# Optimization experiments

Measured on AMD Instinct MI355X. Metric: run time of the kernel, lower is better.

Reference implementation:

```python
import jax, jax.numpy as jnp
import numpy as np

B, FEAT_DIM, GUIDE_DIM, NIR = 1, 128, 128, 33
HL, WL, HH, WH = 64, 64, 256, 256


def make_coord(h, w):
    # pixel-center coords in [-1,1], order (y, x) matching torch make_coord((h,w))
    ys = -1.0 + 1.0 / h + (2.0 / h) * jnp.arange(h, dtype=jnp.float32)
    xs = -1.0 + 1.0 / w + (2.0 / w) * jnp.arange(w, dtype=jnp.float32)
    yy, xx = jnp.meshgrid(ys, xs, indexing='ij')
    return jnp.stack([yy, xx], axis=-1)  # [h, w, 2]


def grid_sample_nearest(img, coord):
    # img [B,C,Hi,Wi]; coord [B,N,2] normalized (y,x).
    # Matches F.grid_sample(mode='nearest', align_corners=False, padding_mode='zeros')
    # (torch passes coord.flip(-1), i.e. (x,y); we index (y,x) directly -- equivalent).
    Bb, C, Hi, Wi = img.shape
    y, x = coord[..., 0], coord[..., 1]
    iy = jnp.round((y + 1.0) * Hi / 2.0 - 0.5).astype(jnp.int32)
    ix = jnp.round((x + 1.0) * Wi / 2.0 - 0.5).astype(jnp.int32)
    valid = (iy >= 0) & (iy < Hi) & (ix >= 0) & (ix < Wi)
    idx = jnp.clip(iy, 0, Hi - 1) * Wi + jnp.clip(ix, 0, Wi - 1)  # [B,N]
    g = jnp.take_along_axis(img.reshape(Bb, C, Hi * Wi), idx[:, None, :], axis=2)
    g = jnp.where(valid[:, None, :], g, 0.0)
    return jnp.transpose(g, (0, 2, 1))  # [B,N,C]


def depthwise3x3(x, k):
    C = x.shape[1]
    return jax.lax.conv_general_dilated(x, k[:, None, :, :], (1, 1), ((1, 1), (1, 1)),
                                        feature_group_count=C,
                                        dimension_numbers=('NCHW', 'OIHW', 'NCHW'))


def query_freq(feat, coord, hr_guide, mlp_fn):
    # local-ensemble implicit decode (query_freq_a / query_freq_p share this skeleton)
    b, c, h, w = feat.shape
    H, W = hr_guide.shape[-2], hr_guide.shape[-1]
    coord = jnp.broadcast_to(coord, (b, H * W, 2))
    fcoord = jnp.broadcast_to(jnp.transpose(make_coord(h, w), (2, 0, 1))[None], (b, 2, h, w))
    q_guide = grid_sample_nearest(hr_guide, coord)  # [b,N,Cg]
    rx, ry = 1.0 / h, 1.0 / w
    hw = jnp.array([float(h), float(w)], dtype=coord.dtype)
    preds = []
    for vx in (-1.0, 1.0):
        for vy in (-1.0, 1.0):
            c_ = coord + jnp.array([vx * rx, vy * ry], dtype=coord.dtype)
            q_feat = grid_sample_nearest(feat, c_)    # [b,N,Cf]
            q_coord = grid_sample_nearest(fcoord, c_)  # [b,N,2]
            rel = (coord - q_coord) * hw
            inp = jnp.concatenate([q_feat, q_guide, rel], axis=-1)  # [b,N,Cin]
            preds.append(mlp_fn(inp, H, W))  # [b,N,NIR]
    preds = jnp.stack(preds, axis=-1)  # [b,N,NIR,4]
    weight = jax.nn.softmax(preds[:, :, -1, :], axis=-1)  # [b,N,4]
    ret = jnp.sum(preds[:, :, :-1, :] * weight[:, :, None, :], axis=-1)  # [b,N,NIR-1]
    return jnp.transpose(ret, (0, 2, 1)).reshape(b, -1, H, W)


def fourier_unit(feat, coord, hr_guide, w1a, b1a, w2a, b2a, w3a, b3a,
                 pw1, dw1, pw2, dw2, pw3, dw3):
    def mlp_a(inp, H, W):  # plain MLP (imnet1)
        x = jax.nn.relu(inp @ w1a + b1a)
        x = jax.nn.relu(x @ w2a + b2a)
        return x @ w3a + b3a

    def mlp_p(inp, H, W):  # conv MLP (imnet2 / MLP_P)
        b = inp.shape[0]
        x = inp.reshape(b, -1, H, W)  # faithful to torch .view on [B,N,Cin]
        x = jax.nn.relu(depthwise3x3(jnp.einsum('bchw,oc->bohw', x, pw1), dw1))
        x = jax.nn.relu(depthwise3x3(jnp.einsum('bchw,oc->bohw', x, pw2), dw2))
        x = depthwise3x3(jnp.einsum('bchw,oc->bohw', x, pw3), dw3)
        return x.reshape(b, H * W, -1)  # faithful to torch .view(B,N,-1)

    feat_f = jnp.fft.fftn(feat, axes=(-2, -1))
    guide_f = jnp.fft.fftn(hr_guide, axes=(-2, -1))
    mag = query_freq(jnp.abs(feat_f), coord, jnp.abs(guide_f), mlp_a)
    pha = query_freq(jnp.angle(feat_f), coord, jnp.angle(guide_f), mlp_p)
    ffted = jax.lax.complex(mag * jnp.cos(pha), mag * jnp.sin(pha))
    return jnp.abs(jnp.fft.ifftn(ffted, axes=(-2, -1)))


def setup_inputs() -> dict:
    key = jax.random.key(0)
    ks = jax.random.split(key, 12)
    cin = FEAT_DIM + GUIDE_DIM + 2  # 258

    def lin(k, i, o):
        return jax.random.normal(k, (i, o), jnp.float32) / np.float32(np.sqrt(i))

    return dict(
        feat=jax.random.normal(ks[0], (B, FEAT_DIM, HL, WL), jnp.float32),
        coord=make_coord(HH, WH).reshape(1, HH * WH, 2),
        hr_guide=jax.random.normal(ks[1], (B, GUIDE_DIM, HH, WH), jnp.float32),
        w1a=lin(ks[2], cin, 256), b1a=jnp.zeros((256,), jnp.float32),
        w2a=lin(ks[3], 256, 128), b2a=jnp.zeros((128,), jnp.float32),
        w3a=lin(ks[4], 128, NIR), b3a=jnp.zeros((NIR,), jnp.float32),
        pw1=jax.random.normal(ks[5], (256, cin), jnp.float32) / np.float32(np.sqrt(cin)),
        dw1=jax.random.normal(ks[6], (256, 3, 3), jnp.float32) / np.float32(3.0),
        pw2=jax.random.normal(ks[7], (128, 256), jnp.float32) / np.float32(16.0),
        dw2=jax.random.normal(ks[8], (128, 3, 3), jnp.float32) / np.float32(3.0),
        pw3=jax.random.normal(ks[9], (NIR, 128), jnp.float32) / np.float32(np.sqrt(128.0)),
        dw3=jax.random.normal(ks[10], (NIR, 3, 3), jnp.float32) / np.float32(3.0),
    )


def reference(feat, coord, hr_guide, w1a, b1a, w2a, b2a, w3a, b3a,
              pw1, dw1, pw2, dw2, pw3, dw3):
    return fourier_unit(feat, coord, hr_guide, w1a, b1a, w2a, b2a, w3a, b3a,
                        pw1, dw1, pw2, dw2, pw3, dw3)
```

## Files before the change

### kernel.cpp

```cpp
#include <hip/hip_runtime.h>
#include <math.h>

typedef __attribute__((ext_vector_type(4))) float f32x4;
typedef __attribute__((ext_vector_type(8))) short bf16x8;
typedef _Float16 f16x8 __attribute__((ext_vector_type(8)));
typedef _Float16 f16x4 __attribute__((ext_vector_type(4)));

__device__ __forceinline__ short f2bf(float v) {
    union { float f; unsigned u; } x; x.f = v;
    unsigned r = x.u + 0x7FFF + ((x.u >> 16) & 1);
    return (short)(r >> 16);
}
__device__ __forceinline__ float bf2f(short b) {
    union { unsigned u; float f; } x; x.u = ((unsigned)(unsigned short)b) << 16;
    return x.f;
}
__device__ __forceinline__ short f2h(float v) {
    union { _Float16 h; short s; } u; u.h = (_Float16)v; return u.s;
}
__device__ __forceinline__ void gload16(const void* g, void* l) {
    __builtin_amdgcn_global_load_lds((const __attribute__((address_space(1))) void*)g,
                                     (__attribute__((address_space(3))) void*)l, 16, 0, 0);
}

template<int N, int MODE>
__global__ __launch_bounds__(256)
void fft_lines(const float* __restrict__ in_real, const float* __restrict__ in_pha,
               const float2* __restrict__ in_c, float2* __restrict__ out_c,
               int nlines, int lpp, int plane_stride, int line_pitch, int stride,
               float sgn, float scale)
{
    constexpr int H = N / 2;
    constexpr int LPB = 256 / H;
    __shared__ float2 bufA[LPB][N];
    __shared__ float2 bufB[LPB][N];
    __shared__ float2 W[H];
    const int tid = threadIdx.x;
    const int sub = tid / H;
    const int b   = tid % H;
    const int L   = blockIdx.x * LPB + sub;
    if (tid < H) {
        float ang = (6.283185307179586f / N) * tid;
        float s, c; sincosf(ang, &s, &c);
        W[tid] = make_float2(c, sgn * s);
    }
    const bool active = (L < nlines);
    size_t base = 0;
    if (active) {
        int p = L / lpp, q = L - p * lpp;
        base = (size_t)p * plane_stride + (size_t)q * line_pitch;
        if (MODE == 0) {
            bufA[sub][b]     = make_float2(in_real[base + (size_t)b * stride], 0.f);
            bufA[sub][b + H] = make_float2(in_real[base + (size_t)(b + H) * stride], 0.f);
        } else if (MODE == 1) {
            bufA[sub][b]     = in_c[base + (size_t)b * stride];
            bufA[sub][b + H] = in_c[base + (size_t)(b + H) * stride];
        } else {
            float m0 = in_real[base + (size_t)b * stride];
            float p0 = in_pha [base + (size_t)b * stride];
            float m1 = in_real[base + (size_t)(b + H) * stride];
            float p1 = in_pha [base + (size_t)(b + H) * stride];
            float s0, c0, s1, c1;
            sincosf(p0, &s0, &c0);
            sincosf(p1, &s1, &c1);
            bufA[sub][b]     = make_float2(m0 * c0, m0 * s0);
            bufA[sub][b + H] = make_float2(m1 * c1, m1 * s1);
        }
    }
    __syncthreads();
    float2 (*X)[N] = bufA;
    float2 (*Y)[N] = bufB;
    int m = 1;
    #pragma unroll
    for (int l = H; l >= 1; l >>= 1) {
        int jm = b & ~(m - 1);
        float2 c0 = X[sub][b];
        float2 c1 = X[sub][b + H];
        float2 w  = W[jm];
        float2 s0 = make_float2(c0.x + c1.x, c0.y + c1.y);
        float2 d  = make_float2(c0.x - c1.x, c0.y - c1.y);
        float2 t  = make_float2(d.x * w.x - d.y * w.y, d.x * w.y + d.y * w.x);
        Y[sub][b + jm]     = s0;
        Y[sub][b + jm + m] = t;
        __syncthreads();
        float2 (*tmp)[N] = X; X = Y; Y = tmp;
        m <<= 1;
    }
    if (active) {
        float2 r0 = X[sub][b], r1 = X[sub][b + H];
        out_c[base + (size_t)b * stride]       = make_float2(r0.x * scale, r0.y * scale);
        out_c[base + (size_t)(b + H) * stride] = make_float2(r1.x * scale, r1.y * scale);
    }
}

template<int N, int TC, int ABSOUT>
__global__ __launch_bounds__(256)
void fft_cols(const float2* __restrict__ in, float2* __restrict__ outc,
              float* __restrict__ outr, float sgn, float scale)
{
    constexpr int Q     = N / 4;
    constexpr int LOG4  = (N == 64) ? 3 : 4;
    constexpr int PITCH = ((N + N / 8 - 8 + 31) / 32) * 32 + 8;
    constexpr int ELD   = (N * TC) / 256;
    constexpr int EBF   = (Q * TC) / 256;
    static_assert((Q * TC) % 256 == 0, "butterfly count must fill block");
    __shared__ float bRe[2][TC * PITCH];
    __shared__ float bIm[2][TC * PITCH];
    __shared__ float Wre[Q + Q / 8 + 1];
    __shared__ float Wim[Q + Q / 8 + 1];
    const int tid = threadIdx.x;
    const int plane = blockIdx.y;
    const int c0 = blockIdx.x * TC;
    const size_t pbase = (size_t)plane * N * N + c0;
    auto lidx = [](int cc, int row) { return cc * PITCH + row + (row >> 3); };

    if (tid < Q) {
        float ang = (6.283185307179586f / N) * tid;
        float s, c; sincosf(ang, &s, &c);
        int wi = tid + (tid >> 3);
        Wre[wi] = c; Wim[wi] = sgn * s;
    }
    #pragma unroll
    for (int e = 0; e < ELD; e++) {
        int q = tid + e * 256;
        int r = q / TC, cc = q % TC;
        float2 v = in[pbase + (size_t)r * N + cc];
        int li = lidx(cc, r);
        bRe[0][li] = v.x; bIm[0][li] = v.y;
    }
    __syncthreads();
    int cur = 0, m = 1;
    #pragma unroll
    for (int stage = 0; stage < LOG4; stage++) {
        #pragma unroll
        for (int e = 0; e < EBF; e++) {
            int idx = tid + e * 256;
            int b = idx % Q, cc = idx / Q;
            int jm = b & ~(m - 1);
            int base = 3 * jm + b;
            int i0 = lidx(cc, b),         i1 = lidx(cc, b + Q);
            int i2 = lidx(cc, b + 2 * Q), i3 = lidx(cc, b + 3 * Q);
            float x0r = bRe[cur][i0], x0i = bIm[cur][i0];
            float x1r = bRe[cur][i1], x1i = bIm[cur][i1];
            float x2r = bRe[cur][i2], x2i = bIm[cur][i2];
            float x3r = bRe[cur][i3], x3i = bIm[cur][i3];
            int wi = jm + (jm >> 3);
            float w1r = Wre[wi], w1i = Wim[wi];
            float w2r = w1r * w1r - w1i * w1i, w2i = 2.f * w1r * w1i;
            float w3r = w2r * w1r - w2i * w1i, w3i = w2r * w1i + w2i * w1r;
            float ar = x0r + x2r, ai = x0i + x2i;
            float br = x0r - x2r, bi = x0i - x2i;
            float cr = x1r + x3r, ci = x1i + x3i;
            float dr = x1r - x3r, di = x1i - x3i;
            float edr = -sgn * di, edi = sgn * dr;
            float y0r = ar + cr,  y0i = ai + ci;
            float y1r = br + edr, y1i = bi + edi;
            float y2r = ar - cr,  y2i = ai - ci;
            float y3r = br - edr, y3i = bi - edi;
            int o0 = lidx(cc, base),         o1 = lidx(cc, base + m);
            int o2 = lidx(cc, base + 2 * m), o3 = lidx(cc, base + 3 * m);
            bRe[cur ^ 1][o0] = y0r;                     bIm[cur ^ 1][o0] = y0i;
            bRe[cur ^ 1][o1] = y1r * w1r - y1i * w1i;   bIm[cur ^ 1][o1] = y1r * w1i + y1i * w1r;
            bRe[cur ^ 1][o2] = y2r * w2r - y2i * w2i;   bIm[cur ^ 1][o2] = y2r * w2i + y2i * w2r;
            bRe[cur ^ 1][o3] = y3r * w3r - y3i * w3i;   bIm[cur ^ 1][o3] = y3r * w3i + y3i * w3r;
        }
        __syncthreads();
        cur ^= 1; m <<= 2;
    }
    #pragma unroll
    for (int e = 0; e < ELD; e++) {
        int q = tid + e * 256;
        int r = q / TC, cc = q % TC;
        int li = lidx(cc, r);
        float vr = bRe[cur][li], vi = bIm[cur][li];
        if (ABSOUT) {
            outr[pbase + (size_t)r * N + cc] = scale * sqrtf(vr * vr + vi * vi);
        } else {
            outc[pbase + (size_t)r * N + cc] = make_float2(vr * scale, vi * scale);
        }
    }
}

__global__ __launch_bounds__(256)
void extract_t(const float2* __restrict__ Fc, short* __restrict__ fAbf,
               short* __restrict__ fPH)
{
    __shared__ float2 T[128][17];
    const int tid = threadIdx.x;
    const int o0 = blockIdx.x * 16;
    #pragma unroll
    for (int e = 0; e < 8; e++) {
        int q = tid + e * 256;
        int c = q >> 4, oo = q & 15;
        T[c][oo] = Fc[(size_t)c * 4096 + o0 + oo];
    }
    __syncthreads();
    #pragma unroll
    for (int e = 0; e < 8; e++) {
        int q = tid + e * 256;
        int oo = q >> 7, c = q & 127;
        float2 v = T[c][oo];
        size_t idx = (size_t)(o0 + oo) * 128 + c;
        fAbf[idx] = f2bf(sqrtf(v.x * v.x + v.y * v.y));
        fPH[idx]  = f2h(atan2f(v.y, v.x));
    }
}

__global__ __launch_bounds__(256)
void gbuild_t(const float2* __restrict__ E, short* __restrict__ Ga,
              short* __restrict__ Gph)
{
    __shared__ float2 T[128][17];
    const int tid = threadIdx.x;
    const int n0 = blockIdx.x * 16;
    #pragma unroll
    for (int e = 0; e < 8; e++) {
        int q = tid + e * 256;
        int c = q >> 4, nn = q & 15;
        T[c][nn] = E[(size_t)c * 65536 + n0 + nn];
    }
    __syncthreads();
    #pragma unroll
    for (int e = 0; e < 8; e++) {
        int q = tid + e * 256;
        int nn = q >> 7, c = q & 127;
        float2 v = T[c][nn];
        size_t o = (size_t)(n0 + nn) * 128 + c;
        Ga[o]  = f2bf(sqrtf(v.x * v.x + v.y * v.y));
        Gph[o] = f2h(atan2f(v.y, v.x));
    }
}

__global__ __launch_bounds__(256)
void mag_h1(const short* __restrict__ FA1, const short* __restrict__ H1g,
            const float* __restrict__ w1a, const float* __restrict__ b1a,
            short* __restrict__ h1, int s0)
{
    int t = blockIdx.x * 256 + threadIdx.x;
    int n = t >> 5, oc = (t & 31) * 8;
    int im = n >> 16, nl = n & 65535;
    int s = s0 + im;
    int oy = (s < 2) ? -3 : 5;
    int ox = (s & 1) ? 5 : -3;
    int i = nl >> 8, jx = nl & 255;
    int iy = (2 * i + oy) >> 3;
    int ix = (2 * jx + ox) >> 3;
    bool valid = (iy >= 0 && iy < 64 && ix >= 0 && ix < 64);
    float ry = valid ? (0.5f * i - 2.f * iy - 0.75f) : (0.5f * i - 63.75f);
    float rx = valid ? (0.5f * jx - 2.f * ix - 0.75f) : (0.5f * jx - 63.75f);
    bf16x8 hv = *(const bf16x8*)&H1g[(size_t)nl * 256 + oc];
    bf16x8 fv = {};
    if (valid) fv = *(const bf16x8*)&FA1[(size_t)(iy * 64 + ix) * 256 + oc];
    bf16x8 out;
    #pragma unroll
    for (int k = 0; k < 8; k++) {
        int o = oc + k;
        float v = b1a[o] + bf2f(hv[k]) + ry * w1a[128 * 256 + o] + rx * w1a[129 * 256 + o];
        if (valid) v += bf2f(fv[k]);
        out[k] = f2bf(fmaxf(v, 0.f));
    }
    *(bf16x8*)&h1[(size_t)n * 256 + oc] = out;
}

__global__ __launch_bounds__(256)
void bphase_tile(const short* __restrict__ featPH, const short* __restrict__ Gph,
                 short* __restrict__ Xp, int s0)
{
    __shared__ short lds[64 * 146];
    const int tid = threadIdx.x;
    const int sh = blockIdx.x >> 11;
    const int inner = blockIdx.x & 2047;
    const int s = s0 + sh;
    const int oy = (s < 2) ? -3 : 5;
    const int ox = (s & 1) ? 5 : -3;
    const int p0 = (inner >> 1) * 64;
    const int half = inner & 1;
    const int pl = tid & 63;
    const int p = p0 + pl;
    const int jq = tid >> 6;
    unsigned* out32 = (unsigned*)Xp + (size_t)sh * 65536 * 144;
    int j = half * 144 + jq;
    unsigned f0 = (unsigned)j * 65536u + (unsigned)p;
    unsigned n = f0 / 258u;
    int c = (int)(f0 - n * 258u);
    #pragma unroll 4
    for (int e = 0; e < 36; e++) {
        short hv = 0;
        if (j < 258) {
            int i = (int)(n >> 8), jx = (int)(n & 255);
            int iy = (2 * i + oy) >> 3;
            int ix = (2 * jx + ox) >> 3;
            bool valid = (iy >= 0 && iy < 64 && ix >= 0 && ix < 64);
            if (c < 128) {
                hv = valid ? featPH[(size_t)(iy * 64 + ix) * 128 + c] : (short)0;
            } else if (c < 256) {
                hv = Gph[(size_t)n * 128 + (c - 128)];
            } else {
                float fv;
                if (c == 256) fv = valid ? (0.5f * i - 2.f * iy - 0.75f) : (0.5f * i - 63.75f);
                else          fv = valid ? (0.5f * jx - 2.f * ix - 0.75f) : (0.5f * jx - 63.75f);
                hv = f2h(fv);
            }
        }
        lds[pl * 146 + (j - half * 144)] = hv;
        j += 4; n += 1016; c += 16;
        if (c >= 258) { c -= 258; n += 1; }
    }
    __syncthreads();
    const unsigned* lds32 = (const unsigned*)lds;
    int pw = tid / 72, dw = tid - pw * 72;
    #pragma unroll 4
    for (int e = 0; e < 18; e++) {
        out32[(size_t)(p0 + pw) * 144 + half * 72 + dw] = lds32[pw * 73 + dw];
        pw += 3; dw += 40;
        if (dw >= 72) { dw -= 72; pw += 1; }
    }
}

__global__ void wprep_T(const float* __restrict__ src, short* __restrict__ dst,
                        int Ncols, int Nd, int Kp, int k0, int kn, int kr0, int krn)
{
    int t = blockIdx.x * 256 + threadIdx.x;
    if (t >= Nd * Kp) return;
    int o = t / Kp, j = t - o * Kp;
    int c = (j < kn) ? (k0 + j) : ((j < kn + krn) ? (kr0 + j - kn) : -1);
    float v = 0.f;
    if (c >= 0 && o < Ncols) v = src[(size_t)c * Ncols + o];
    dst[t] = f2bf(v);
}
__global__ void wprep_f16(const float* __restrict__ src, short* __restrict__ dst,
                          int Nsrc, int Ksrc, int Nd, int Kp, int kn)
{
    int t = blockIdx.x * 256 + threadIdx.x;
    if (t >= Nd * Kp) return;
    int o = t / Kp, j = t - o * Kp;
    float v = 0.f;
    if (j < kn && o < Nsrc) v = src[(size_t)o * Ksrc + j];
    dst[t] = f2h(v);
}

template<int RELU, int BIAS, int CIN, int OUTT, int F16>
__global__ __launch_bounds__(256)
void gemm_mfma(const short* __restrict__ A, const short* __restrict__ Bt,
               const float* __restrict__ bias, const void* __restrict__ Cin,
               void* __restrict__ Cout,
               int K, int Apitch, int Bpitch, int ldc, int Nout)
{
    __shared__ short As[4096];
    __shared__ short Bs[4096];
    const int tid = threadIdx.x;
    const int wave = tid >> 6, lane = tid & 63;
    const int bm = blockIdx.y * 128, bn = blockIdx.x * 128;
    const int wr = wave >> 1, wc = wave & 1;
    const int srow = wave * 32 + (lane >> 2);
    const int scol = (lane & 3) * 8;
    const int ldsoff = srow * 32 + scol;
    f32x4 acc[4][4] = {};
    const int ks_n = K >> 5;
    for (int ks = 0; ks < ks_n; ks++) {
        const int k0 = ks << 5;
        const short* gA = A + (size_t)(bm + srow) * Apitch + k0 + scol;
        gload16(gA, &As[ldsoff]);
        gload16(gA + 16 * Apitch, &As[ldsoff + 512]);
        const short* gB = Bt + (size_t)(bn + srow) * Bpitch + k0 + scol;
        gload16(gB, &Bs[ldsoff]);
        gload16(gB + 16 * Bpitch, &Bs[ldsoff + 512]);
        __syncthreads();
        const int fr = lane & 15;
        const int kreg = (lane >> 4) << 3;
        bf16x8 ah[4], bh[4];
        #pragma unroll
        for (int m = 0; m < 4; m++)
            ah[m] = *(const bf16x8*)&As[(wr * 64 + m * 16 + fr) * 32 + kreg];
        #pragma unroll
        for (int n = 0; n < 4; n++)
            bh[n] = *(const bf16x8*)&Bs[(wc * 64 + n * 16 + fr) * 32 + kreg];
        #pragma unroll
        for (int m = 0; m < 4; m++)
            #pragma unroll
            for (int n = 0; n < 4; n++) {
                if constexpr (F16)
                    acc[m][n] = __builtin_amdgcn_mfma_f32_16x16x32_f16(
                        __builtin_bit_cast(f16x8, ah[m]),
                        __builtin_bit_cast(f16x8, bh[n]), acc[m][n], 0, 0, 0);
                else
                    acc[m][n] = __builtin_amdgcn_mfma_f32_16x16x32_bf16(
                        ah[m], bh[n], acc[m][n], 0, 0, 0);
            }
        __syncthreads();
    }
    const int fr = lane & 15;
    const int rg = (lane >> 4) * 4;
    #pragma unroll
    for (int n = 0; n < 4; n++) {
        const int col = bn + wc * 64 + n * 16 + fr;
        if (col >= Nout) continue;
        const float bv = BIAS ? bias[col] : 0.f;
        #pragma unroll
        for (int m = 0; m < 4; m++) {
            const int row0 = bm + wr * 64 + m * 16 + rg;
            #pragma unroll
            for (int r = 0; r < 4; r++) {
                float v = acc[m][n][r] + bv;
                const size_t ci = (size_t)(row0 + r) * ldc + col;
                if (CIN == 1) v += bf2f(((const short*)Cin)[ci]);
                if (RELU) v = fmaxf(v, 0.f);
                if constexpr (OUTT == 1)      ((float*)Cout)[ci] = v;
                else if constexpr (OUTT == 2) ((_Float16*)Cout)[ci] = (_Float16)v;
                else                          ((short*)Cout)[ci] = f2bf(v);
            }
        }
    }
}

template<int C, int RELU>
__global__ __launch_bounds__(256)
void dwconv_f16(const _Float16* __restrict__ in, const float* __restrict__ w,
                _Float16* __restrict__ out)
{
    constexpr int CG = C / 4;
    constexpr int SUBS = 256 / CG;
    constexpr int PX = SUBS * 2;
    const int tid = threadIdx.x;
    const int cg = tid % CG;
    const int c4 = cg * 4;
    const int sub = tid / CG;
    const int p0 = blockIdx.x * PX + sub * 2;
    const int im = p0 >> 16;
    const int pl = p0 & 65535;
    const int y = pl >> 8, x0 = pl & 255;
    const size_t ibase = (size_t)im * 65536 * C;
    float wk[4][9];
    #pragma unroll
    for (int k = 0; k < 4; k++)
        #pragma unroll
        for (int q = 0; q < 9; q++) wk[k][q] = w[(c4 + k) * 9 + q];
    f16x4 v[3][4];
    #pragma unroll
    for (int dy = 0; dy < 3; dy++) {
        int yy = y + dy - 1;
        bool yv = (yy >= 0) && (yy <= 255);
        int yc = min(max(yy, 0), 255);
        #pragma unroll
        for (int dx = 0; dx < 4; dx++) {
            int xx = x0 + dx - 1;
            bool xv = (xx >= 0) && (xx <= 255);
            int xc = min(max(xx, 0), 255);
            f16x4 t = *(const f16x4*)&in[ibase + (size_t)(yc * 256 + xc) * C + c4];
            v[dy][dx] = (yv && xv) ? t : (f16x4){};
        }
    }
    float a0[4] = {}, a1[4] = {};
    #pragma unroll
    for (int dy = 0; dy < 3; dy++)
        #pragma unroll
        for (int dx = 0; dx < 3; dx++)
            #pragma unroll
            for (int k = 0; k < 4; k++) {
                a0[k] += (float)v[dy][dx][k]     * wk[k][dy * 3 + dx];
                a1[k] += (float)v[dy][dx + 1][k] * wk[k][dy * 3 + dx];
            }
    f16x4 o0, o1;
    #pragma unroll
    for (int k = 0; k < 4; k++) {
        float b0 = RELU ? fmaxf(a0[k], 0.f) : a0[k];
        float b1 = RELU ? fmaxf(a1[k], 0.f) : a1[k];
        o0[k] = (_Float16)b0;
        o1[k] = (_Float16)b1;
    }
    *(f16x4*)&out[(size_t)p0 * C + c4]       = o0;
    *(f16x4*)&out[(size_t)(p0 + 1) * C + c4] = o1;
}

__global__ __launch_bounds__(256)
void dwconv3_t(const float* __restrict__ in, const float* __restrict__ w,
               float* __restrict__ out)
{
    __shared__ float lds[33][65];
    const int tid = threadIdx.x;
    const int im = blockIdx.x >> 10;
    const int inner = blockIdx.x & 1023;
    const int y = inner >> 2;
    const int x0 = (inner & 3) * 64;
    const size_t ibase = (size_t)im * 65536 * 33;
    const size_t obase = (size_t)im * 65536 * 33;
    #pragma unroll
    for (int e = 0; e < 9; e++) {
        int q = e * 256 + tid;
        if (q < 2112) {
            int x = q / 33, c = q - x * 33;
            float acc = 0.f;
            #pragma unroll
            for (int dy = 0; dy < 3; dy++) {
                int yy = y + dy - 1;
                bool yv = (yy >= 0) && (yy <= 255);
                int yc = min(max(yy, 0), 255);
                #pragma unroll
                for (int dx = 0; dx < 3; dx++) {
                    int xx = x0 + x + dx - 1;
                    bool xv = (xx >= 0) && (xx <= 255);
                    int xc = min(max(xx, 0), 255);
                    float t = in[ibase + (size_t)(yc * 256 + xc) * 33 + c];
                    acc += ((yv && xv) ? t : 0.f) * w[c * 9 + dy * 3 + dx];
                }
            }
            lds[c][x] = acc;
        }
    }
    __syncthreads();
    const int xx = tid & 63, c4 = tid >> 6;
    #pragma unroll
    for (int cg = 0; cg < 36; cg += 4) {
        int cc = cg + c4;
        if (cc < 33)
            out[obase + (size_t)cc * 65536 + y * 256 + x0 + xx] = lds[cc][xx];
    }
}

__global__ __launch_bounds__(256)
void ensemble_a(const short* __restrict__ P, float* __restrict__ mag)
{
    int n = blockIdx.x * 256 + threadIdx.x;
    float w[4]; float mx = -1e30f;
    #pragma unroll
    for (int s = 0; s < 4; s++) {
        w[s] = bf2f(P[((size_t)s * 65536 + n) * 33 + 32]);
        mx = fmaxf(mx, w[s]);
    }
    float sum = 0.f;
    #pragma unroll
    for (int s = 0; s < 4; s++) { w[s] = expf(w[s] - mx); sum += w[s]; }
    float inv = 1.f / sum;
    for (int ch = 0; ch < 32; ch++) {
        float a = 0.f;
        #pragma unroll
        for (int s = 0; s < 4; s++)
            a += bf2f(P[((size_t)s * 65536 + n) * 33 + ch]) * w[s];
        mag[(size_t)ch * 65536 + n] = a * inv;
    }
}

__global__ __launch_bounds__(256)
void ensemble_p(const float* __restrict__ P, float* __restrict__ pha)
{
    const size_t SOFF = (size_t)65536 * 33;
    int n = blockIdx.x * 256 + threadIdx.x;
    const size_t base = (size_t)n * 33;
    float w[4]; float mx = -1e30f;
    #pragma unroll
    for (int s = 0; s < 4; s++) {
        w[s] = P[(size_t)s * SOFF + base + 32];
        mx = fmaxf(mx, w[s]);
    }
    float sum = 0.f;
    #pragma unroll
    for (int s = 0; s < 4; s++) { w[s] = expf(w[s] - mx); sum += w[s]; }
    float inv = 1.f / sum;
    for (int jj = 0; jj < 32; jj++) {
        float a = 0.f;
        #pragma unroll
        for (int s = 0; s < 4; s++)
            a += P[(size_t)s * SOFF + base + jj] * w[s];
        pha[(size_t)jj * 65536 + n] = a * inv;
    }
}

extern "C" void kernel_launch(void* const* d_in, const int* in_sizes, int n_in,
                              void* d_out, int out_size, void* d_ws, size_t ws_size,
                              hipStream_t stream)
{
    (void)in_sizes; (void)n_in; (void)out_size; (void)ws_size;
    const float* feat = (const float*)d_in[0];
    const float* hr   = (const float*)d_in[2];
    const float* w1a  = (const float*)d_in[3];
    const float* b1a  = (const float*)d_in[4];
    const float* w2a  = (const float*)d_in[5];
    const float* b2a  = (const float*)d_in[6];
    const float* w3a  = (const float*)d_in[7];
    const float* b3a  = (const float*)d_in[8];
    const float* pw1  = (const float*)d_in[9];
    const float* dw1  = (const float*)d_in[10];
    const float* pw2  = (const float*)d_in[11];
    const float* dw2  = (const float*)d_in[12];
    const float* pw3  = (const float*)d_in[13];
    const float* dw3  = (const float*)d_in[14];

    char* W = (char*)d_ws;
    const size_t oA = 0;
    const size_t oB = 75497472;
    const size_t oC = oB + 67108864;
    const size_t oD = oC + 33554432;
    const size_t oM = oD + 34603008;
    const size_t oF = oM + 12582912;
    const size_t oN = oF + 786432;

    float2* E     = (float2*)(W + oA);
    short*  h1_2  = (short*) (W + oA);
    short*  Xp2   = (short*) (W + oA);
    _Float16* X2_2 = (_Float16*)(W + oA);
    float*  C3_2  = (float*) (W + oA);
    float*  Hp    = (float*) (W + oA);
    float2* Fc    = (float2*)(W + oB);
    short*  Ga    = (short*) (W + oB);
    short*  h2_2  = (short*) (W + oB);
    short*  H1g   = (short*) (W + oB + 33554432);
    _Float16* C1_2 = (_Float16*)(W + oB);
    _Float16* C2_2 = (_Float16*)(W + oB);
    _Float16* X3_2 = (_Float16*)(W + oB + 33554432);
    float2* Z     = (float2*)(W + oB);
    short*  Gph   = (short*) (W + oC);
    short*  PA    = (short*) (W + oD);
    float*  PP    = (float*) (W + oD);
    short*  featPH = (short*)(W + oM);
    float*  Hm     = (float*)(W + oM + 4194304);
    short* W1g = (short*)(W + oF + 81920);
    short* W2  = (short*)(W + oF + 147456);
    short* W3  = (short*)(W + oF + 212992);
    short* Pf  = (short*)(W + oF + 245760);
    short* P2  = (short*)(W + oF + 393216);
    short* P3  = (short*)(W + oF + 458752);
    short* W1a128 = (short*)(W + oF + 491520);
    short* featAbf = (short*)(W + oN);
    short* FA1     = (short*)(W + oN + 1048576);

    const size_t SOFF = (size_t)65536 * 33;

    wprep_T<<<128, 256, 0, stream>>>(w1a, W1a128, 256, 256, 128, 0, 128, 0, 0);
    wprep_T<<<128, 256, 0, stream>>>(w1a, W1g, 256, 256, 128, 128, 128, 0, 0);
    wprep_T<<<128, 256, 0, stream>>>(w2a, W2, 128, 128, 256, 0, 256, 0, 0);
    wprep_T<<<64,  256, 0, stream>>>(w3a, W3, 33, 128, 128, 0, 128, 0, 0);
    wprep_f16<<<288, 256, 0, stream>>>(pw1, Pf, 256, 258, 256, 288, 258);
    wprep_f16<<<128, 256, 0, stream>>>(pw2, P2, 128, 256, 128, 256, 256);
    wprep_f16<<<64,  256, 0, stream>>>(pw3, P3, 33, 128, 128, 128, 128);

    fft_lines<256, 0><<<16384, 256, 0, stream>>>(hr, nullptr, nullptr, E, 32768, 256, 65536, 256, 1, -1.f, 1.f);
    fft_cols<256, 8, 0><<<dim3(32, 128), 256, 0, stream>>>(E, E, nullptr, -1.f, 1.f);
    fft_lines<64, 0><<<1024, 256, 0, stream>>>(feat, nullptr, nullptr, Fc, 8192, 64, 4096, 64, 1, -1.f, 1.f);
    fft_cols<64, 16, 0><<<dim3(4, 128), 256, 0, stream>>>(Fc, Fc, nullptr, -1.f, 1.f);
    extract_t<<<256, 256, 0, stream>>>(Fc, featAbf, featPH);

    gbuild_t<<<4096, 256, 0, stream>>>(E, Ga, Gph);

    gemm_mfma<0,0,0,0,0><<<dim3(2,512), 256, 0, stream>>>(Ga, W1g, nullptr, nullptr, H1g, 128, 128, 128, 256, 256);
    gemm_mfma<0,0,0,0,0><<<dim3(2,32), 256, 0, stream>>>(featAbf, W1a128, nullptr, nullptr, FA1, 128, 128, 128, 256, 256);

    for (int s0 = 0; s0 < 4; s0 += 2) {
        mag_h1<<<16384, 256, 0, stream>>>(FA1, H1g, w1a, b1a, h1_2, s0);
        gemm_mfma<1,1,0,0,0><<<dim3(1,1024), 256, 0, stream>>>(h1_2, W2, b2a, nullptr, h2_2, 256, 256, 256, 128, 128);
        gemm_mfma<0,1,0,0,0><<<dim3(1,1024), 256, 0, stream>>>(h2_2, W3, b3a, nullptr, PA + (size_t)s0 * SOFF, 128, 128, 128, 33, 33);
    }
    ensemble_a<<<256, 256, 0, stream>>>(PA, Hm);

    for (int s0 = 0; s0 < 4; s0 += 2) {
        bphase_tile<<<4096, 256, 0, stream>>>(featPH, Gph, Xp2, s0);
        gemm_mfma<0,0,0,2,1><<<dim3(2,1024), 256, 0, stream>>>(Xp2, Pf, nullptr, nullptr, C1_2, 288, 288, 288, 256, 256);
        dwconv_f16<256,1><<<16384, 256, 0, stream>>>(C1_2, dw1, X2_2);
        gemm_mfma<0,0,0,2,1><<<dim3(1,1024), 256, 0, stream>>>((const short*)X2_2, P2, nullptr, nullptr, C2_2, 256, 256, 256, 128, 128);
        dwconv_f16<128,1><<<8192, 256, 0, stream>>>(C2_2, dw2, X3_2);
        gemm_mfma<0,0,0,1,1><<<dim3(1,1024), 256, 0, stream>>>((const short*)X3_2, P3, nullptr, nullptr, C3_2, 128, 128, 128, 33, 33);
        dwconv3_t<<<2048, 256, 0, stream>>>(C3_2, dw3, PP + (size_t)s0 * SOFF);
    }
    ensemble_p<<<256, 256, 0, stream>>>(PP, Hp);

    fft_lines<256, 2><<<4096, 256, 0, stream>>>(Hm, Hp, nullptr, Z, 8192, 256, 65536, 256, 1, 1.f, 1.f / 256.f);
    fft_cols<256, 8, 1><<<dim3(32, 32), 256, 0, stream>>>(Z, nullptr, (float*)d_out, 1.f, 1.f / 256.f);
}
```

Measured before the change: 768.8 us.

## Fuse A-operand construction of mag and phase MLPs into GEMM prologue

Removes the separate mag_h1 and bphase_tile kernels. The gemm_mfma template now builds its A tiles directly in LDS from FA1/H1g (bias, coordinate terms, ReLU) or from featPH/Gph (gathered phase features plus relative coordinates). This avoids writing and re-reading the large intermediate h1 and Xp buffers. In exchange, the GEMM load path becomes scalar gather plus compute, which cannot use async global_load_lds. The phase path may also recompute the gather for each of the two column blocks.

```diff
diff --git a/kernel.cpp b/kernel.cpp
--- a/kernel.cpp
+++ b/kernel.cpp
@@ -231,92 +231,6 @@
     }
 }
 
-__global__ __launch_bounds__(256)
-void mag_h1(const short* __restrict__ FA1, const short* __restrict__ H1g,
-            const float* __restrict__ w1a, const float* __restrict__ b1a,
-            short* __restrict__ h1, int s0)
-{
-    int t = blockIdx.x * 256 + threadIdx.x;
-    int n = t >> 5, oc = (t & 31) * 8;
-    int im = n >> 16, nl = n & 65535;
-    int s = s0 + im;
-    int oy = (s < 2) ? -3 : 5;
-    int ox = (s & 1) ? 5 : -3;
-    int i = nl >> 8, jx = nl & 255;
-    int iy = (2 * i + oy) >> 3;
-    int ix = (2 * jx + ox) >> 3;
-    bool valid = (iy >= 0 && iy < 64 && ix >= 0 && ix < 64);
-    float ry = valid ? (0.5f * i - 2.f * iy - 0.75f) : (0.5f * i - 63.75f);
-    float rx = valid ? (0.5f * jx - 2.f * ix - 0.75f) : (0.5f * jx - 63.75f);
-    bf16x8 hv = *(const bf16x8*)&H1g[(size_t)nl * 256 + oc];
-    bf16x8 fv = {};
-    if (valid) fv = *(const bf16x8*)&FA1[(size_t)(iy * 64 + ix) * 256 + oc];
-    bf16x8 out;
-    #pragma unroll
-    for (int k = 0; k < 8; k++) {
-        int o = oc + k;
-        float v = b1a[o] + bf2f(hv[k]) + ry * w1a[128 * 256 + o] + rx * w1a[129 * 256 + o];
-        if (valid) v += bf2f(fv[k]);
-        out[k] = f2bf(fmaxf(v, 0.f));
-    }
-    *(bf16x8*)&h1[(size_t)n * 256 + oc] = out;
-}
-
-__global__ __launch_bounds__(256)
-void bphase_tile(const short* __restrict__ featPH, const short* __restrict__ Gph,
-                 short* __restrict__ Xp, int s0)
-{
-    __shared__ short lds[64 * 146];
-    const int tid = threadIdx.x;
-    const int sh = blockIdx.x >> 11;
-    const int inner = blockIdx.x & 2047;
-    const int s = s0 + sh;
-    const int oy = (s < 2) ? -3 : 5;
-    const int ox = (s & 1) ? 5 : -3;
-    const int p0 = (inner >> 1) * 64;
-    const int half = inner & 1;
-    const int pl = tid & 63;
-    const int p = p0 + pl;
-    const int jq = tid >> 6;
-    unsigned* out32 = (unsigned*)Xp + (size_t)sh * 65536 * 144;
-    int j = half * 144 + jq;
-    unsigned f0 = (unsigned)j * 65536u + (unsigned)p;
-    unsigned n = f0 / 258u;
-    int c = (int)(f0 - n * 258u);
-    #pragma unroll 4
-    for (int e = 0; e < 36; e++) {
-        short hv = 0;
-        if (j < 258) {
-            int i = (int)(n >> 8), jx = (int)(n & 255);
-            int iy = (2 * i + oy) >> 3;
-            int ix = (2 * jx + ox) >> 3;
-            bool valid = (iy >= 0 && iy < 64 && ix >= 0 && ix < 64);
-            if (c < 128) {
-                hv = valid ? featPH[(size_t)(iy * 64 + ix) * 128 + c] : (short)0;
-            } else if (c < 256) {
-                hv = Gph[(size_t)n * 128 + (c - 128)];
-            } else {
-                float fv;
-                if (c == 256) fv = valid ? (0.5f * i - 2.f * iy - 0.75f) : (0.5f * i - 63.75f);
-                else          fv = valid ? (0.5f * jx - 2.f * ix - 0.75f) : (0.5f * jx - 63.75f);
-                hv = f2h(fv);
-            }
-        }
-        lds[pl * 146 + (j - half * 144)] = hv;
-        j += 4; n += 1016; c += 16;
-        if (c >= 258) { c -= 258; n += 1; }
-    }
-    __syncthreads();
-    const unsigned* lds32 = (const unsigned*)lds;
-    int pw = tid / 72, dw = tid - pw * 72;
-    #pragma unroll 4
-    for (int e = 0; e < 18; e++) {
-        out32[(size_t)(p0 + pw) * 144 + half * 72 + dw] = lds32[pw * 73 + dw];
-        pw += 3; dw += 40;
-        if (dw >= 72) { dw -= 72; pw += 1; }
-    }
-}
-
 __global__ void wprep_T(const float* __restrict__ src, short* __restrict__ dst,
                         int Ncols, int Nd, int Kp, int k0, int kn, int kr0, int krn)
 {
@@ -339,12 +253,15 @@
     dst[t] = f2h(v);
 }
 
-template<int RELU, int BIAS, int CIN, int OUTT, int F16>
+template<int RELU, int BIAS, int CIN, int OUTT, int F16, int STAGEA = 0>
 __global__ __launch_bounds__(256)
 void gemm_mfma(const short* __restrict__ A, const short* __restrict__ Bt,
                const float* __restrict__ bias, const void* __restrict__ Cin,
                void* __restrict__ Cout,
-               int K, int Apitch, int Bpitch, int ldc, int Nout)
+               int K, int Apitch, int Bpitch, int ldc, int Nout,
+               const void* __restrict__ aux0, const void* __restrict__ aux1,
+               const float* __restrict__ aux2, const float* __restrict__ aux3,
+               int s0)
 {
     __shared__ short As[4096];
     __shared__ short Bs[4096];
@@ -357,11 +274,115 @@
     const int ldsoff = srow * 32 + scol;
     f32x4 acc[4][4] = {};
     const int ks_n = K >> 5;
+
+    int sg_oy = 0, sg_ox = 0;
+    unsigned sg_n0 = 0, sg_n1 = 0; int sg_c0 = 0, sg_c1 = 0;
+    int sg_cell0 = 0, sg_cell1 = 0; bool sg_v0 = false, sg_v1 = false;
+    float sg_ry0 = 0, sg_rx0 = 0, sg_ry1 = 0, sg_rx1 = 0;
+    if constexpr (STAGEA != 0) {
+        int sh = bm >> 16;
+        int s = s0 + sh;
+        sg_oy = (s < 2) ? -3 : 5;
+        sg_ox = (s & 1) ? 5 : -3;
+        #pragma unroll
+        for (int rr = 0; rr < 2; rr++) {
+            int r = bm + srow + rr * 16;
+            int nl = r & 65535;
+            if constexpr (STAGEA == 1) {
+                unsigned f0 = (unsigned)scol * 65536u + (unsigned)nl;
+                unsigned nn = f0 / 258u;
+                int cc = (int)(f0 - nn * 258u);
+                if (rr == 0) { sg_n0 = nn; sg_c0 = cc; } else { sg_n1 = nn; sg_c1 = cc; }
+            } else {
+                int i = nl >> 8, jx = nl & 255;
+                int iy = (2 * i + sg_oy) >> 3;
+                int ix = (2 * jx + sg_ox) >> 3;
+                bool valid = (iy >= 0 && iy < 64 && ix >= 0 && ix < 64);
+                float ry = valid ? (0.5f * i - 2.f * iy - 0.75f) : (0.5f * i - 63.75f);
+                float rx = valid ? (0.5f * jx - 2.f * ix - 0.75f) : (0.5f * jx - 63.75f);
+                int cell = iy * 64 + ix;
+                if (rr == 0) { sg_cell0 = cell; sg_v0 = valid; sg_ry0 = ry; sg_rx0 = rx; }
+                else         { sg_cell1 = cell; sg_v1 = valid; sg_ry1 = ry; sg_rx1 = rx; }
+            }
+        }
+    }
+
     for (int ks = 0; ks < ks_n; ks++) {
         const int k0 = ks << 5;
-        const short* gA = A + (size_t)(bm + srow) * Apitch + k0 + scol;
-        gload16(gA, &As[ldsoff]);
-        gload16(gA + 16 * Apitch, &As[ldsoff + 512]);
+        if constexpr (STAGEA == 0) {
+            const short* gA = A + (size_t)(bm + srow) * Apitch + k0 + scol;
+            gload16(gA, &As[ldsoff]);
+            gload16(gA + 16 * Apitch, &As[ldsoff + 512]);
+        } else if constexpr (STAGEA == 1) {
+            const short* fPH = (const short*)aux0;
+            const short* GpH = (const short*)aux1;
+            #pragma unroll
+            for (int rr = 0; rr < 2; rr++) {
+                unsigned nn = rr ? sg_n1 : sg_n0;
+                int cc = rr ? sg_c1 : sg_c0;
+                int jj = k0 + scol;
+                bf16x8 hv8 = {};
+                #pragma unroll
+                for (int e = 0; e < 8; e++) {
+                    short hv = 0;
+                    if (jj < 258) {
+                        int i = (int)(nn >> 8), jx = (int)(nn & 255);
+                        int iy = (2 * i + sg_oy) >> 3;
+                        int ix = (2 * jx + sg_ox) >> 3;
+                        bool valid = (iy >= 0 && iy < 64 && ix >= 0 && ix < 64);
+                        if (cc < 128) {
+                            hv = valid ? fPH[(size_t)(iy * 64 + ix) * 128 + cc] : (short)0;
+                        } else if (cc < 256) {
+                            hv = GpH[(size_t)nn * 128 + (cc - 128)];
+                        } else {
+                            float fv;
+                            if (cc == 256) fv = valid ? (0.5f * i - 2.f * iy - 0.75f) : (0.5f * i - 63.75f);
+                            else           fv = valid ? (0.5f * jx - 2.f * ix - 0.75f) : (0.5f * jx - 63.75f);
+                            hv = f2h(fv);
+                        }
+                    }
+                    hv8[e] = hv;
+                    jj++; nn += 254; cc += 4;
+                    if (cc >= 258) { cc -= 258; nn += 1; }
+                }
+                *(bf16x8*)&As[ldsoff + rr * 512] = hv8;
+                if (rr == 0) { sg_n0 += 8128; sg_c0 += 128; if (sg_c0 >= 258) { sg_c0 -= 258; sg_n0 += 1; } }
+                else         { sg_n1 += 8128; sg_c1 += 128; if (sg_c1 >= 258) { sg_c1 -= 258; sg_n1 += 1; } }
+            }
+        } else {
+            const short* FA1p = (const short*)aux0;
+            const short* H1gp = (const short*)aux1;
+            const int o0 = k0 + scol;
+            f32x4 bva = *(const f32x4*)&aux3[o0];
+            f32x4 bvb = *(const f32x4*)&aux3[o0 + 4];
+            f32x4 wya = *(const f32x4*)&aux2[128 * 256 + o0];
+            f32x4 wyb = *(const f32x4*)&aux2[128 * 256 + o0 + 4];
+            f32x4 wxa = *(const f32x4*)&aux2[129 * 256 + o0];
+            f32x4 wxb = *(const f32x4*)&aux2[129 * 256 + o0 + 4];
+            #pragma unroll
+            for (int rr = 0; rr < 2; rr++) {
+                int r = bm + srow + rr * 16;
+                int nl = r & 65535;
+                bool valid = rr ? sg_v1 : sg_v0;
+                int cell = rr ? sg_cell1 : sg_cell0;
+                float ry = rr ? sg_ry1 : sg_ry0;
+                float rx = rr ? sg_rx1 : sg_rx0;
+                bf16x8 hv = *(const bf16x8*)&H1gp[(size_t)nl * 256 + o0];
+                bf16x8 fv = {};
+                if (valid) fv = *(const bf16x8*)&FA1p[(size_t)cell * 256 + o0];
+                bf16x8 out8;
+                #pragma unroll
+                for (int e = 0; e < 8; e++) {
+                    float b = (e < 4) ? bva[e] : bvb[e - 4];
+                    float wy = (e < 4) ? wya[e] : wyb[e - 4];
+                    float wx = (e < 4) ? wxa[e] : wxb[e - 4];
+                    float v = b + bf2f(hv[e]) + ry * wy + rx * wx;
+                    if (valid) v += bf2f(fv[e]);
+                    out8[e] = f2bf(fmaxf(v, 0.f));
+                }
+                *(bf16x8*)&As[ldsoff + rr * 512] = out8;
+            }
+        }
         const short* gB = Bt + (size_t)(bn + srow) * Bpitch + k0 + scol;
         gload16(gB, &Bs[ldsoff]);
         gload16(gB + 16 * Bpitch, &Bs[ldsoff + 512]);
@@ -595,8 +616,6 @@
     const size_t oN = oF + 786432;
 
     float2* E     = (float2*)(W + oA);
-    short*  h1_2  = (short*) (W + oA);
-    short*  Xp2   = (short*) (W + oA);
     _Float16* X2_2 = (_Float16*)(W + oA);
     float*  C3_2  = (float*) (W + oA);
     float*  Hp    = (float*) (W + oA);
@@ -641,23 +660,21 @@
 
     gbuild_t<<<4096, 256, 0, stream>>>(E, Ga, Gph);
 
-    gemm_mfma<0,0,0,0,0><<<dim3(2,512), 256, 0, stream>>>(Ga, W1g, nullptr, nullptr, H1g, 128, 128, 128, 256, 256);
-    gemm_mfma<0,0,0,0,0><<<dim3(2,32), 256, 0, stream>>>(featAbf, W1a128, nullptr, nullptr, FA1, 128, 128, 128, 256, 256);
+    gemm_mfma<0,0,0,0,0,0><<<dim3(2,512), 256, 0, stream>>>(Ga, W1g, nullptr, nullptr, H1g, 128, 128, 128, 256, 256, nullptr, nullptr, nullptr, nullptr, 0);
+    gemm_mfma<0,0,0,0,0,0><<<dim3(2,32), 256, 0, stream>>>(featAbf, W1a128, nullptr, nullptr, FA1, 128, 128, 128, 256, 256, nullptr, nullptr, nullptr, nullptr, 0);
 
     for (int s0 = 0; s0 < 4; s0 += 2) {
-        mag_h1<<<16384, 256, 0, stream>>>(FA1, H1g, w1a, b1a, h1_2, s0);
-        gemm_mfma<1,1,0,0,0><<<dim3(1,1024), 256, 0, stream>>>(h1_2, W2, b2a, nullptr, h2_2, 256, 256, 256, 128, 128);
-        gemm_mfma<0,1,0,0,0><<<dim3(1,1024), 256, 0, stream>>>(h2_2, W3, b3a, nullptr, PA + (size_t)s0 * SOFF, 128, 128, 128, 33, 33);
+        gemm_mfma<1,1,0,0,0,2><<<dim3(1,1024), 256, 0, stream>>>(nullptr, W2, b2a, nullptr, h2_2, 256, 0, 256, 128, 128, FA1, H1g, w1a, b1a, s0);
+        gemm_mfma<0,1,0,0,0,0><<<dim3(1,1024), 256, 0, stream>>>(h2_2, W3, b3a, nullptr, PA + (size_t)s0 * SOFF, 128, 128, 128, 33, 33, nullptr, nullptr, nullptr, nullptr, 0);
     }
     ensemble_a<<<256, 256, 0, stream>>>(PA, Hm);
 
     for (int s0 = 0; s0 < 4; s0 += 2) {
-        bphase_tile<<<4096, 256, 0, stream>>>(featPH, Gph, Xp2, s0);
-        gemm_mfma<0,0,0,2,1><<<dim3(2,1024), 256, 0, stream>>>(Xp2, Pf, nullptr, nullptr, C1_2, 288, 288, 288, 256, 256);
+        gemm_mfma<0,0,0,2,1,1><<<dim3(2,1024), 256, 0, stream>>>(nullptr, Pf, nullptr, nullptr, C1_2, 288, 0, 288, 256, 256, featPH, Gph, nullptr, nullptr, s0);
         dwconv_f16<256,1><<<16384, 256, 0, stream>>>(C1_2, dw1, X2_2);
-        gemm_mfma<0,0,0,2,1><<<dim3(1,1024), 256, 0, stream>>>((const short*)X2_2, P2, nullptr, nullptr, C2_2, 256, 256, 256, 128, 128);
+        gemm_mfma<0,0,0,2,1,0><<<dim3(1,1024), 256, 0, stream>>>((const short*)X2_2, P2, nullptr, nullptr, C2_2, 256, 256, 256, 128, 128, nullptr, nullptr, nullptr, nullptr, 0);
         dwconv_f16<128,1><<<8192, 256, 0, stream>>>(C2_2, dw2, X3_2);
-        gemm_mfma<0,0,0,1,1><<<dim3(1,1024), 256, 0, stream>>>((const short*)X3_2, P3, nullptr, nullptr, C3_2, 128, 128, 128, 33, 33);
+        gemm_mfma<0,0,0,1,1,0><<<dim3(1,1024), 256, 0, stream>>>((const short*)X3_2, P3, nullptr, nullptr, C3_2, 128, 128, 128, 33, 33, nullptr, nullptr, nullptr, nullptr, 0);
         dwconv3_t<<<2048, 256, 0, stream>>>(C3_2, dw3, PP + (size_t)s0 * SOFF);
     }
     ensemble_p<<<256, 256, 0, stream>>>(PP, Hp);
```

Measured after the change: 942.8 us. 1.23x slower.
